# Performance work log

Hardware: AMD Instinct MI355X
Metric: run time of the kernel (lower is better)

Reference implementation:

```python
import jax, jax.numpy as jnp
import numpy as np

N_NODES = 50000
N_EDGES = 1600000
IN_DIM = 512
OUT_DIM = 256


def setup_inputs() -> dict:
    key = jax.random.key(0)
    k1, k2, k3, k4, k5, k6 = jax.random.split(key, 6)
    inputs = jax.random.normal(k1, (N_NODES, IN_DIM), dtype=jnp.float32)
    edge_row = jax.random.randint(k2, (N_EDGES,), 0, N_NODES, dtype=jnp.int32)
    edge_col = jax.random.randint(k3, (N_EDGES,), 0, N_NODES, dtype=jnp.int32)
    edge_val = jax.random.uniform(k4, (N_EDGES,), dtype=jnp.float32)
    stdv = 1.0 / np.sqrt(OUT_DIM)
    weight = jax.random.uniform(k5, (IN_DIM, OUT_DIM), dtype=jnp.float32, minval=-stdv, maxval=stdv)
    bias = jax.random.uniform(k6, (OUT_DIM,), dtype=jnp.float32, minval=-stdv, maxval=stdv)
    return {"inputs": inputs, "edge_row": edge_row, "edge_col": edge_col,
            "edge_val": edge_val, "weight": weight, "bias": bias}


def reference(inputs, edge_row, edge_col, edge_val, weight, bias):
    # dense GEMM: [N, in] @ [in, out] -> [N, out]
    support = inputs @ weight
    # SpMM: out[r] += val * support[c] for each edge (r, c, val)
    gathered = edge_val[:, None] * support[edge_col]  # [E, out]
    output = jax.ops.segment_sum(gathered, edge_row, num_segments=N_NODES)
    return output + bias
```

## Files before the change

kernel.cpp:

```cpp
#include <hip/hip_runtime.h>

#define N_NODES 50000
#define N_EDGES 1600000
#define IN_DIM 512
#define OUT_DIM 256

#define BM 128
#define BN 128
#define BK 32
#define APAD 8
#define LDA (BK + APAD)

#define RPB   128
#define NBKT  391
#define CHUNK 4096
#define CAP   5120

typedef unsigned int u32;
typedef unsigned short u16;
typedef short bf16x8 __attribute__((ext_vector_type(8)));
typedef float f32x4 __attribute__((ext_vector_type(4)));

__device__ __forceinline__ float bf_to_f(u16 u) { return __uint_as_float(((u32)u) << 16); }
__device__ __forceinline__ u16 f_to_bf(float f) {
    u32 u = __float_as_uint(f);
    u32 r = (u + 0x7fffu + ((u >> 16) & 1u)) >> 16;
    return (u16)r;
}

__global__ __launch_bounds__(256) void zero_cur(int* __restrict__ cursor) {
    const int i = blockIdx.x * 256 + threadIdx.x;
    if (i < NBKT) cursor[i] = 0;
}

__global__ __launch_bounds__(256) void scatter1(const int* __restrict__ er,
                                                const int* __restrict__ ec,
                                                const float* __restrict__ ev,
                                                int* __restrict__ cursor,
                                                int2* __restrict__ tmp) {
    __shared__ int  hcnt[NBKT];
    __shared__ int  loff[NBKT];
    __shared__ int  gbase[NBKT];
    __shared__ int  sc[512];
    __shared__ int2 estage[CHUNK];
    __shared__ u16  bslot[CHUNK];

    const int t = threadIdx.x;
    const int base = blockIdx.x * CHUNK;
    const int nedge = min(CHUNK, N_EDGES - base);

    for (int k = t; k < NBKT; k += 256) hcnt[k] = 0;
    __syncthreads();

    int w0[16], w1[16], rk[16];
    #pragma unroll
    for (int j = 0; j < 16; ++j) {
        const int i = j * 256 + t;
        rk[j] = -1;
        if (i < nedge) {
            const int e = base + i;
            const int r = er[e];
            const int bk = r >> 7;
            w0[j] = ec[e] | ((r & 127) << 16) | (bk << 23);
            w1[j] = __float_as_int(ev[e]);
            rk[j] = atomicAdd(&hcnt[bk], 1);
        }
    }
    __syncthreads();

    sc[t]       = (t < NBKT) ? hcnt[t] : 0;
    sc[t + 256] = (t + 256 < NBKT) ? hcnt[t + 256] : 0;
    __syncthreads();
    #pragma unroll
    for (int off = 1; off < 512; off <<= 1) {
        const int a0 = (t >= off) ? sc[t - off] : 0;
        const int a1 = sc[t + 256 - off];
        __syncthreads();
        sc[t] += a0;
        sc[t + 256] += a1;
        __syncthreads();
    }
    if (t < NBKT)       loff[t]       = sc[t] - hcnt[t];
    if (t + 256 < NBKT) loff[t + 256] = sc[t + 256] - hcnt[t + 256];

    if (t < NBKT && hcnt[t] > 0)
        gbase[t] = t * CAP + atomicAdd(&cursor[t], hcnt[t]);
    if (t + 256 < NBKT && hcnt[t + 256] > 0)
        gbase[t + 256] = (t + 256) * CAP + atomicAdd(&cursor[t + 256], hcnt[t + 256]);
    __syncthreads();

    #pragma unroll
    for (int j = 0; j < 16; ++j) {
        if (rk[j] >= 0) {
            const int bk = ((u32)w0[j]) >> 23;
            const int s = loff[bk] + rk[j];
            estage[s] = make_int2(w0[j], w1[j]);
            bslot[s]  = (u16)bk;
        }
    }
    __syncthreads();

    for (int s = t; s < nedge; s += 256) {
        const int bk = bslot[s];
        const int2 e2 = estage[s];
        const int gpos = gbase[bk] + (s - loff[bk]);
        if (gpos < (bk + 1) * CAP)
            tmp[gpos] = e2;
    }
}

__global__ __launch_bounds__(256) void bscan(const int* __restrict__ cursor,
                                             int* __restrict__ bucket_base,
                                             int* __restrict__ row_ptr) {
    __shared__ int sc[512];
    __shared__ int orig[512];
    const int t = threadIdx.x;
    const int c0 = (t < NBKT) ? min(cursor[t], CAP) : 0;
    const int c1 = (t + 256 < NBKT) ? min(cursor[t + 256], CAP) : 0;
    sc[t] = c0;       orig[t] = c0;
    sc[t + 256] = c1; orig[t + 256] = c1;
    __syncthreads();
    #pragma unroll
    for (int off = 1; off < 512; off <<= 1) {
        const int a0 = (t >= off) ? sc[t - off] : 0;
        const int a1 = sc[t + 256 - off];
        __syncthreads();
        sc[t] += a0;
        sc[t + 256] += a1;
        __syncthreads();
    }
    if (t < NBKT)       bucket_base[t]       = sc[t] - orig[t];
    if (t + 256 < NBKT) bucket_base[t + 256] = sc[t + 256] - orig[t + 256];
    if (t == 0) row_ptr[N_NODES] = N_EDGES;
}

__global__ __launch_bounds__(256) void scatter2(const int* __restrict__ cursor,
                                                const int* __restrict__ bucket_base,
                                                const int2* __restrict__ tmp,
                                                int* __restrict__ row_ptr,
                                                int2* __restrict__ sedge) {
    __shared__ int rcnt[RPB];
    __shared__ int sc[RPB];
    __shared__ int rcur[RPB];
    const int t = threadIdx.x;
    const int b = blockIdx.x;
    const int n = min(cursor[b], CAP);
    const int2* src = tmp + (size_t)b * CAP;
    const int gb = bucket_base[b];

    if (t < RPB) rcnt[t] = 0;
    __syncthreads();
    for (int i = t; i < n; i += 256)
        atomicAdd(&rcnt[(((u32)src[i].x) >> 16) & 127], 1);
    __syncthreads();

    if (t < RPB) sc[t] = rcnt[t];
    __syncthreads();
    #pragma unroll
    for (int off = 1; off < RPB; off <<= 1) {
        int a = 0;
        if (t < RPB && t >= off) a = sc[t - off];
        __syncthreads();
        if (t < RPB) sc[t] += a;
        __syncthreads();
    }
    if (t < RPB) {
        const int excl = sc[t] - rcnt[t];
        rcur[t] = gb + excl;
        const int row = b * RPB + t;
        if (row < N_NODES) row_ptr[row] = gb + excl;
    }
    __syncthreads();

    for (int i = t; i < n; i += 256) {
        const int2 e2 = src[i];
        const int rloc = (((u32)e2.x) >> 16) & 127;
        const int pos = atomicAdd(&rcur[rloc], 1);
        sedge[pos] = make_int2(e2.x & 0xFFFF, e2.y);
    }
}

__global__ __launch_bounds__(256) void wcvt(const float* __restrict__ W,
                                            u16* __restrict__ WT) {
    const int n  = threadIdx.x;
    const int k0 = blockIdx.x * 4;
    ushort4 o;
    o.x = f_to_bf(W[(size_t)(k0 + 0) * OUT_DIM + n]);
    o.y = f_to_bf(W[(size_t)(k0 + 1) * OUT_DIM + n]);
    o.z = f_to_bf(W[(size_t)(k0 + 2) * OUT_DIM + n]);
    o.w = f_to_bf(W[(size_t)(k0 + 3) * OUT_DIM + n]);
    *(ushort4*)(WT + (size_t)n * IN_DIM + k0) = o;
}

__global__ __launch_bounds__(256) void gemm_mfma(const float* __restrict__ X,
                                                 const u16* __restrict__ WT,
                                                 u16* __restrict__ Sb) {
    __shared__ u16 As[BM * LDA];
    __shared__ u16 Bs[BN * LDA];

    const int tid  = threadIdx.x;
    const int wave = tid >> 6;
    const int lane = tid & 63;
    const int r0   = blockIdx.x * BM;
    const int n0   = blockIdx.y * BN;
    const int wm   = (wave & 1) * 64;
    const int wn   = (wave >> 1) * 64;
    const int l15  = lane & 15;
    const int quad = lane >> 4;

    f32x4 acc[4][4];
    #pragma unroll
    for (int i = 0; i < 4; ++i)
        #pragma unroll
        for (int j = 0; j < 4; ++j) acc[i][j] = (f32x4)0.f;

    const int srow = tid >> 1;
    const int skp  = (tid & 1) * 16;
    const int xrow = min(r0 + srow, N_NODES - 1);
    const float* xsrc = X + (size_t)xrow * IN_DIM + skp;
    const u16*   bsrc = WT + (size_t)(n0 + srow) * IN_DIM + skp;

    for (int kc = 0; kc < IN_DIM; kc += BK) {
        {
            const float4 f0 = *(const float4*)(xsrc + kc + 0);
            const float4 f1 = *(const float4*)(xsrc + kc + 4);
            const float4 f2 = *(const float4*)(xsrc + kc + 8);
            const float4 f3 = *(const float4*)(xsrc + kc + 12);
            ushort4 p0, p1, p2, p3;
            p0.x = f_to_bf(f0.x); p0.y = f_to_bf(f0.y); p0.z = f_to_bf(f0.z); p0.w = f_to_bf(f0.w);
            p1.x = f_to_bf(f1.x); p1.y = f_to_bf(f1.y); p1.z = f_to_bf(f1.z); p1.w = f_to_bf(f1.w);
            p2.x = f_to_bf(f2.x); p2.y = f_to_bf(f2.y); p2.z = f_to_bf(f2.z); p2.w = f_to_bf(f2.w);
            p3.x = f_to_bf(f3.x); p3.y = f_to_bf(f3.y); p3.z = f_to_bf(f3.z); p3.w = f_to_bf(f3.w);
            *(ushort4*)&As[srow * LDA + skp + 0]  = p0;
            *(ushort4*)&As[srow * LDA + skp + 4]  = p1;
            *(ushort4*)&As[srow * LDA + skp + 8]  = p2;
            *(ushort4*)&As[srow * LDA + skp + 12] = p3;
        }
        {
            const uint4 b0 = *(const uint4*)(bsrc + kc);
            const uint4 b1 = *(const uint4*)(bsrc + kc + 8);
            *(uint4*)&Bs[srow * LDA + skp + 0] = b0;
            *(uint4*)&Bs[srow * LDA + skp + 8] = b1;
        }
        __syncthreads();

        bf16x8 af[4], bfr[4];
        #pragma unroll
        for (int mt = 0; mt < 4; ++mt)
            af[mt] = *(const bf16x8*)&As[(wm + mt * 16 + l15) * LDA + quad * 8];
        #pragma unroll
        for (int nt = 0; nt < 4; ++nt)
            bfr[nt] = *(const bf16x8*)&Bs[(wn + nt * 16 + l15) * LDA + quad * 8];
        #pragma unroll
        for (int mt = 0; mt < 4; ++mt)
            #pragma unroll
            for (int nt = 0; nt < 4; ++nt)
                acc[mt][nt] = __builtin_amdgcn_mfma_f32_16x16x32_bf16(
                    af[mt], bfr[nt], acc[mt][nt], 0, 0, 0);
        __syncthreads();
    }

    #pragma unroll
    for (int mt = 0; mt < 4; ++mt) {
        #pragma unroll
        for (int r = 0; r < 4; ++r) {
            const int grow = r0 + wm + mt * 16 + quad * 4 + r;
            if (grow < N_NODES) {
                u16* dst = Sb + (size_t)grow * OUT_DIM + n0 + wn + l15;
                #pragma unroll
                for (int nt = 0; nt < 4; ++nt)
                    dst[nt * 16] = f_to_bf(acc[mt][nt][r]);
            }
        }
    }
}

__global__ __launch_bounds__(256) void csr_spmm(const int* __restrict__ row_ptr,
                                                const int2* __restrict__ sedge,
                                                const u16* __restrict__ Sb,
                                                const float* __restrict__ bias,
                                                float* __restrict__ out) {
    const int wave = threadIdx.x >> 6;
    const int lane = threadIdx.x & 63;
    const int r = blockIdx.x * 4 + wave;
    if (r >= N_NODES) return;

    const int start = row_ptr[r];
    const int end   = row_ptr[r + 1];

    float4 acc = *(const float4*)(bias + lane * 4);
    const u16* sbase = Sb + lane * 4;

    for (int e = start; e < end; e += 8) {
        int2 ed[8];
        #pragma unroll
        for (int j = 0; j < 8; ++j) {
            const int idx = min(e + j, end - 1);
            ed[j] = sedge[idx];
        }
        #pragma unroll
        for (int j = 0; j < 8; ++j)
            if (e + j >= end) ed[j].y = 0;

        ushort4 sv[8];
        #pragma unroll
        for (int j = 0; j < 8; ++j)
            sv[j] = *(const ushort4*)(sbase + (size_t)ed[j].x * OUT_DIM);

        #pragma unroll
        for (int j = 0; j < 8; ++j) {
            const float vj = __int_as_float(ed[j].y);
            acc.x += vj * bf_to_f(sv[j].x);
            acc.y += vj * bf_to_f(sv[j].y);
            acc.z += vj * bf_to_f(sv[j].z);
            acc.w += vj * bf_to_f(sv[j].w);
        }
    }

    *(float4*)(out + (size_t)r * OUT_DIM + lane * 4) = acc;
}

extern "C" void kernel_launch(void* const* d_in, const int* in_sizes, int n_in,
                              void* d_out, int out_size, void* d_ws, size_t ws_size,
                              hipStream_t stream) {
    const float* X    = (const float*)d_in[0];
    const int*   er   = (const int*)d_in[1];
    const int*   ec   = (const int*)d_in[2];
    const float* ev   = (const float*)d_in[3];
    const float* W    = (const float*)d_in[4];
    const float* bias = (const float*)d_in[5];
    float* out        = (float*)d_out;

    char* ws = (char*)d_ws;
    u16*  Sb      = (u16*) (ws);
    int2* tmp     = (int2*)(ws);
    int*  cursor  = (int*) (ws + 16100000);
    int*  bbase   = (int*) (ws + 16110000);
    int2* sedge   = (int2*)(ws + 25600000);
    u16*  WT      = (u16*) (ws + 38400000);
    int*  row_ptr = (int*) (ws + 38662144);

    hipLaunchKernelGGL(zero_cur, dim3(2), dim3(256), 0, stream, cursor);
    hipLaunchKernelGGL(scatter1, dim3((N_EDGES + CHUNK - 1) / CHUNK), dim3(256), 0,
                       stream, er, ec, ev, cursor, tmp);
    hipLaunchKernelGGL(bscan, dim3(1), dim3(256), 0, stream, cursor, bbase, row_ptr);
    hipLaunchKernelGGL(scatter2, dim3(NBKT), dim3(256), 0, stream,
                       cursor, bbase, tmp, row_ptr, sedge);
    hipLaunchKernelGGL(wcvt, dim3(IN_DIM / 4), dim3(256), 0, stream, W, WT);
    hipLaunchKernelGGL(gemm_mfma, dim3((N_NODES + BM - 1) / BM, OUT_DIM / BN),
                       dim3(256), 0, stream, X, WT, Sb);
    hipLaunchKernelGGL(csr_spmm, dim3((N_NODES + 3) / 4), dim3(256), 0, stream,
                       row_ptr, sedge, Sb, bias, out);
}
```

Before: 359.2 us.

## Store support in column-chunked layout and split SpMM across feature chunks

The GEMM now writes the bf16 support matrix as 8 column chunks of 32 features, each chunk stored contiguously over all nodes. The SpMM launches 8 blocks per group of 8 rows, one per chunk, with each half-wave handling one row and one feature per lane. Each chunk of the gathered matrix is about 3.2 MB, so concurrent blocks on the same chunk should hit in L2 more often. In exchange, edge indices are re-read once per chunk, each gather is a 2-byte scalar load instead of an 8-byte vector, and rows sharing a wave run to the larger of the two degrees.

```diff
diff --git a/kernel.cpp b/kernel.cpp
--- a/kernel.cpp
+++ b/kernel.cpp
@@ -15,6 +15,9 @@
 #define NBKT  391
 #define CHUNK 4096
 #define CAP   5120
+
+#define CH     32
+#define NCHUNK 8
 
 typedef unsigned int u32;
 typedef unsigned short u16;
@@ -194,7 +197,7 @@
 
 __global__ __launch_bounds__(256) void gemm_mfma(const float* __restrict__ X,
                                                  const u16* __restrict__ WT,
-                                                 u16* __restrict__ Sb) {
+                                                 u16* __restrict__ Sbc) {
     __shared__ u16 As[BM * LDA];
     __shared__ u16 Bs[BN * LDA];
 
@@ -266,58 +269,59 @@
         for (int r = 0; r < 4; ++r) {
             const int grow = r0 + wm + mt * 16 + quad * 4 + r;
             if (grow < N_NODES) {
-                u16* dst = Sb + (size_t)grow * OUT_DIM + n0 + wn + l15;
                 #pragma unroll
-                for (int nt = 0; nt < 4; ++nt)
-                    dst[nt * 16] = f_to_bf(acc[mt][nt][r]);
+                for (int nt = 0; nt < 4; ++nt) {
+                    const int col = n0 + wn + nt * 16 + l15;
+                    Sbc[((size_t)(col >> 5) * N_NODES + grow) * CH + (col & 31)]
+                        = f_to_bf(acc[mt][nt][r]);
+                }
             }
         }
     }
 }
 
-__global__ __launch_bounds__(256) void csr_spmm(const int* __restrict__ row_ptr,
-                                                const int2* __restrict__ sedge,
-                                                const u16* __restrict__ Sb,
-                                                const float* __restrict__ bias,
-                                                float* __restrict__ out) {
-    const int wave = threadIdx.x >> 6;
-    const int lane = threadIdx.x & 63;
-    const int r = blockIdx.x * 4 + wave;
-    if (r >= N_NODES) return;
+__global__ __launch_bounds__(256) void spmm_chunked(const int* __restrict__ row_ptr,
+                                                    const int2* __restrict__ sedge,
+                                                    const u16* __restrict__ Sbc,
+                                                    const float* __restrict__ bias,
+                                                    float* __restrict__ out) {
+    const int bid   = blockIdx.x;
+    const int chunk = bid & 7;
+    const int rg    = bid >> 3;
+    const int wave  = threadIdx.x >> 6;
+    const int lane  = threadIdx.x & 63;
+    const int ch    = lane & 31;
+    const int half  = lane >> 5;
+    const int r     = rg * 8 + wave * 2 + half;
 
     const int start = row_ptr[r];
-    const int end   = row_ptr[r + 1];
-
-    float4 acc = *(const float4*)(bias + lane * 4);
-    const u16* sbase = Sb + lane * 4;
-
-    for (int e = start; e < end; e += 8) {
-        int2 ed[8];
+    const int deg   = row_ptr[r + 1] - start;
+    const int mdeg  = max(deg, __shfl_xor(deg, 32));
+
+    const u16* sb = Sbc + (size_t)chunk * (N_NODES * CH) + ch;
+    const long long* se = (const long long*)sedge;
+    float acc = bias[chunk * CH + ch];
+
+    for (int i = 0; i < mdeg; i += 8) {
+        int   cols[8];
+        float vals[8];
         #pragma unroll
         for (int j = 0; j < 8; ++j) {
-            const int idx = min(e + j, end - 1);
-            ed[j] = sedge[idx];
-        }
+            const int idx = min(start + i + j, N_EDGES - 1);
+            const long long ed = __builtin_nontemporal_load(se + idx);
+            cols[j] = (int)(u32)ed;
+            vals[j] = (i + j < deg) ? __int_as_float((int)(ed >> 32)) : 0.f;
+        }
+        u16 sv[8];
         #pragma unroll
         for (int j = 0; j < 8; ++j)
-            if (e + j >= end) ed[j].y = 0;
-
-        ushort4 sv[8];
+            sv[j] = sb[(size_t)cols[j] * CH];
         #pragma unroll
         for (int j = 0; j < 8; ++j)
-            sv[j] = *(const ushort4*)(sbase + (size_t)ed[j].x * OUT_DIM);
-
-        #pragma unroll
-        for (int j = 0; j < 8; ++j) {
-            const float vj = __int_as_float(ed[j].y);
-            acc.x += vj * bf_to_f(sv[j].x);
-            acc.y += vj * bf_to_f(sv[j].y);
-            acc.z += vj * bf_to_f(sv[j].z);
-            acc.w += vj * bf_to_f(sv[j].w);
-        }
-    }
-
-    *(float4*)(out + (size_t)r * OUT_DIM + lane * 4) = acc;
+            acc += vals[j] * bf_to_f(sv[j]);
+    }
+
+    __builtin_nontemporal_store(acc, out + (size_t)r * OUT_DIM + chunk * CH + ch);
 }
 
 extern "C" void kernel_launch(void* const* d_in, const int* in_sizes, int n_in,
@@ -332,7 +336,7 @@
     float* out        = (float*)d_out;
 
     char* ws = (char*)d_ws;
-    u16*  Sb      = (u16*) (ws);
+    u16*  Sbc     = (u16*) (ws);
     int2* tmp     = (int2*)(ws);
     int*  cursor  = (int*) (ws + 16100000);
     int*  bbase   = (int*) (ws + 16110000);
@@ -348,7 +352,7 @@
                        cursor, bbase, tmp, row_ptr, sedge);
     hipLaunchKernelGGL(wcvt, dim3(IN_DIM / 4), dim3(256), 0, stream, W, WT);
     hipLaunchKernelGGL(gemm_mfma, dim3((N_NODES + BM - 1) / BM, OUT_DIM / BN),
-                       dim3(256), 0, stream, X, WT, Sb);
-    hipLaunchKernelGGL(csr_spmm, dim3((N_NODES + 3) / 4), dim3(256), 0, stream,
-                       row_ptr, sedge, Sb, bias, out);
-}
+                       dim3(256), 0, stream, X, WT, Sbc);
+    hipLaunchKernelGGL(spmm_chunked, dim3(8 * (N_NODES / 8)), dim3(256), 0, stream,
+                       row_ptr, sedge, Sbc, bias, out);
+}
```

After: 603.7 us. 68.1% more time.

## Widen GEMM tile to full output width and use nontemporal SpMM edge loads

Applied to the files above, without the earlier changes.

The GEMM block now covers all 256 output columns with 512 threads and 8 waves, so each block reads and converts its X tile once instead of twice across two column blocks. This halves the global reads of the fp32 input and the bf16 conversion work. The SpMM kernel loads edges with nontemporal 64-bit loads, folds the tail masking into the load loop, and writes the output with nontemporal stores so streaming data does not evict the gathered support rows from cache. Larger blocks use more registers and LDS per block, which may lower occupancy.

```diff
diff --git a/kernel.cpp b/kernel.cpp
--- a/kernel.cpp
+++ b/kernel.cpp
@@ -6,7 +6,7 @@
 #define OUT_DIM 256
 
 #define BM 128
-#define BN 128
+#define BN 256
 #define BK 32
 #define APAD 8
 #define LDA (BK + APAD)
@@ -192,7 +192,7 @@
     *(ushort4*)(WT + (size_t)n * IN_DIM + k0) = o;
 }
 
-__global__ __launch_bounds__(256) void gemm_mfma(const float* __restrict__ X,
+__global__ __launch_bounds__(512) void gemm_mfma(const float* __restrict__ X,
                                                  const u16* __restrict__ WT,
                                                  u16* __restrict__ Sb) {
     __shared__ u16 As[BM * LDA];
@@ -202,7 +202,6 @@
     const int wave = tid >> 6;
     const int lane = tid & 63;
     const int r0   = blockIdx.x * BM;
-    const int n0   = blockIdx.y * BN;
     const int wm   = (wave & 1) * 64;
     const int wn   = (wave >> 1) * 64;
     const int l15  = lane & 15;
@@ -214,33 +213,29 @@
         #pragma unroll
         for (int j = 0; j < 4; ++j) acc[i][j] = (f32x4)0.f;
 
-    const int srow = tid >> 1;
-    const int skp  = (tid & 1) * 16;
-    const int xrow = min(r0 + srow, N_NODES - 1);
-    const float* xsrc = X + (size_t)xrow * IN_DIM + skp;
-    const u16*   bsrc = WT + (size_t)(n0 + srow) * IN_DIM + skp;
+    const int arow = tid >> 2;
+    const int akp  = (tid & 3) * 8;
+    const int xrow = min(r0 + arow, N_NODES - 1);
+    const float* xsrc = X + (size_t)xrow * IN_DIM + akp;
+    const int brow = tid >> 1;
+    const int bkp  = (tid & 1) * 16;
+    const u16* bsrc = WT + (size_t)brow * IN_DIM + bkp;
 
     for (int kc = 0; kc < IN_DIM; kc += BK) {
         {
             const float4 f0 = *(const float4*)(xsrc + kc + 0);
             const float4 f1 = *(const float4*)(xsrc + kc + 4);
-            const float4 f2 = *(const float4*)(xsrc + kc + 8);
-            const float4 f3 = *(const float4*)(xsrc + kc + 12);
-            ushort4 p0, p1, p2, p3;
+            ushort4 p0, p1;
             p0.x = f_to_bf(f0.x); p0.y = f_to_bf(f0.y); p0.z = f_to_bf(f0.z); p0.w = f_to_bf(f0.w);
             p1.x = f_to_bf(f1.x); p1.y = f_to_bf(f1.y); p1.z = f_to_bf(f1.z); p1.w = f_to_bf(f1.w);
-            p2.x = f_to_bf(f2.x); p2.y = f_to_bf(f2.y); p2.z = f_to_bf(f2.z); p2.w = f_to_bf(f2.w);
-            p3.x = f_to_bf(f3.x); p3.y = f_to_bf(f3.y); p3.z = f_to_bf(f3.z); p3.w = f_to_bf(f3.w);
-            *(ushort4*)&As[srow * LDA + skp + 0]  = p0;
-            *(ushort4*)&As[srow * LDA + skp + 4]  = p1;
-            *(ushort4*)&As[srow * LDA + skp + 8]  = p2;
-            *(ushort4*)&As[srow * LDA + skp + 12] = p3;
+            *(ushort4*)&As[arow * LDA + akp + 0] = p0;
+            *(ushort4*)&As[arow * LDA + akp + 4] = p1;
         }
         {
             const uint4 b0 = *(const uint4*)(bsrc + kc);
             const uint4 b1 = *(const uint4*)(bsrc + kc + 8);
-            *(uint4*)&Bs[srow * LDA + skp + 0] = b0;
-            *(uint4*)&Bs[srow * LDA + skp + 8] = b1;
+            *(uint4*)&Bs[brow * LDA + bkp + 0] = b0;
+            *(uint4*)&Bs[brow * LDA + bkp + 8] = b1;
         }
         __syncthreads();
 
@@ -266,7 +261,7 @@
         for (int r = 0; r < 4; ++r) {
             const int grow = r0 + wm + mt * 16 + quad * 4 + r;
             if (grow < N_NODES) {
-                u16* dst = Sb + (size_t)grow * OUT_DIM + n0 + wn + l15;
+                u16* dst = Sb + (size_t)grow * OUT_DIM + wn + l15;
                 #pragma unroll
                 for (int nt = 0; nt < 4; ++nt)
                     dst[nt * 16] = f_to_bf(acc[mt][nt][r]);
@@ -290,34 +285,38 @@
 
     float4 acc = *(const float4*)(bias + lane * 4);
     const u16* sbase = Sb + lane * 4;
+    const long long* se = (const long long*)sedge;
 
     for (int e = start; e < end; e += 8) {
-        int2 ed[8];
+        int   cols[8];
+        float vals[8];
         #pragma unroll
         for (int j = 0; j < 8; ++j) {
             const int idx = min(e + j, end - 1);
-            ed[j] = sedge[idx];
-        }
+            const long long ed = __builtin_nontemporal_load(se + idx);
+            cols[j] = (int)(u32)ed;
+            vals[j] = (e + j < end) ? __int_as_float((int)(ed >> 32)) : 0.f;
+        }
+
+        ushort4 sv[8];
         #pragma unroll
         for (int j = 0; j < 8; ++j)
-            if (e + j >= end) ed[j].y = 0;
-
-        ushort4 sv[8];
-        #pragma unroll
-        for (int j = 0; j < 8; ++j)
-            sv[j] = *(const ushort4*)(sbase + (size_t)ed[j].x * OUT_DIM);
+            sv[j] = *(const ushort4*)(sbase + (size_t)cols[j] * OUT_DIM);
 
         #pragma unroll
         for (int j = 0; j < 8; ++j) {
-            const float vj = __int_as_float(ed[j].y);
-            acc.x += vj * bf_to_f(sv[j].x);
-            acc.y += vj * bf_to_f(sv[j].y);
-            acc.z += vj * bf_to_f(sv[j].z);
-            acc.w += vj * bf_to_f(sv[j].w);
-        }
-    }
-
-    *(float4*)(out + (size_t)r * OUT_DIM + lane * 4) = acc;
+            acc.x += vals[j] * bf_to_f(sv[j].x);
+            acc.y += vals[j] * bf_to_f(sv[j].y);
+            acc.z += vals[j] * bf_to_f(sv[j].z);
+            acc.w += vals[j] * bf_to_f(sv[j].w);
+        }
+    }
+
+    float* dst = out + (size_t)r * OUT_DIM + lane * 4;
+    __builtin_nontemporal_store(acc.x, dst + 0);
+    __builtin_nontemporal_store(acc.y, dst + 1);
+    __builtin_nontemporal_store(acc.z, dst + 2);
+    __builtin_nontemporal_store(acc.w, dst + 3);
 }
 
 extern "C" void kernel_launch(void* const* d_in, const int* in_sizes, int n_in,
@@ -347,8 +346,8 @@
     hipLaunchKernelGGL(scatter2, dim3(NBKT), dim3(256), 0, stream,
                        cursor, bbase, tmp, row_ptr, sedge);
     hipLaunchKernelGGL(wcvt, dim3(IN_DIM / 4), dim3(256), 0, stream, W, WT);
-    hipLaunchKernelGGL(gemm_mfma, dim3((N_NODES + BM - 1) / BM, OUT_DIM / BN),
-                       dim3(256), 0, stream, X, WT, Sb);
+    hipLaunchKernelGGL(gemm_mfma, dim3((N_NODES + BM - 1) / BM), dim3(512), 0,
+                       stream, X, WT, Sb);
     hipLaunchKernelGGL(csr_spmm, dim3((N_NODES + 3) / 4), dim3(256), 0, stream,
                        row_ptr, sedge, Sb, bias, out);
 }
```

Measured after the change: 376.3 us. +4.8%, slower.
